# Performance work log

Measured on AMD Instinct MI355X. Metric: run time of the kernel, lower is better.

The kernel has to match this reference:

```python
import jax, jax.numpy as jnp
import numpy as np

N_NODES = 50000
N_EDGES = 800000
QRY = 128
KEY = 128
VAL = 128
HEADS = 8
HEAD_FEATS = VAL // HEADS
BN_EPS = 1e-5


def setup_inputs() -> dict:
    key = jax.random.key(0)
    ks = jax.random.split(key, 12)
    inp = {
        "ft_q": jax.random.normal(ks[0], (N_NODES, QRY), dtype=jnp.float32),
        "ft_k": jax.random.normal(ks[1], (N_NODES, KEY), dtype=jnp.float32),
        "src": jax.random.randint(ks[2], (N_EDGES,), 0, N_NODES, dtype=jnp.int32),
        "dst": jax.random.randint(ks[3], (N_EDGES,), 0, N_NODES, dtype=jnp.int32),
        # learned params
        "Wq": jax.random.normal(ks[4], (VAL, QRY), dtype=jnp.float32) / np.sqrt(QRY),
        "bq": jnp.zeros((VAL,), dtype=jnp.float32),
        "Wk": jax.random.normal(ks[5], (VAL, KEY), dtype=jnp.float32) / np.sqrt(KEY),
        "Wv": jax.random.normal(ks[6], (VAL, QRY), dtype=jnp.float32) / np.sqrt(QRY),
        "attn_e": jax.random.normal(ks[7], (VAL,), dtype=jnp.float32),
        "bn_q_g": jnp.ones((QRY,), dtype=jnp.float32),
        "bn_q_b": jnp.zeros((QRY,), dtype=jnp.float32),
        "bn_k_g": jnp.ones((KEY,), dtype=jnp.float32),
        "bn_k_b": jnp.zeros((KEY,), dtype=jnp.float32),
    }
    return inp


def _batch_norm(x, gamma, beta):
    # training-mode BatchNorm1d: normalize over batch dim
    mean = jnp.mean(x, axis=0, keepdims=True)
    var = jnp.var(x, axis=0, keepdims=True)
    return (x - mean) * jax.lax.rsqrt(var + BN_EPS) * gamma + beta


def reference(ft_q, ft_k, src, dst, Wq, bq, Wk, Wv, attn_e,
              bn_q_g, bn_q_b, bn_k_g, bn_k_b):
    ft_q = _batch_norm(ft_q, bn_q_g, bn_q_b)
    ft_k = _batch_norm(ft_k, bn_k_g, bn_k_b)

    q = ft_q @ Wq.T + bq                      # [N, VAL]
    k = ft_k @ Wk.T                           # [N, VAL]
    v = (ft_q @ Wv.T).reshape(-1, HEADS, HEAD_FEATS)  # [N, H, D]

    # u_add_v: per-edge e = q[src] + k[dst]
    e = q[src] + k[dst]                       # [E, VAL]
    e = (attn_e * jax.nn.sigmoid(e)).reshape(-1, HEADS, HEAD_FEATS).sum(-1)  # [E, H]

    # edge_softmax grouped by destination node
    m = jax.ops.segment_max(e, dst, num_segments=N_NODES)   # [N, H]
    ex = jnp.exp(e - m[dst])                                # [E, H]
    s = jax.ops.segment_sum(ex, dst, num_segments=N_NODES)  # [N, H]
    a = ex / s[dst]                                         # [E, H]

    # u_mul_e_sum: scatter-sum of v[src] * a over destination
    msg = v[src] * a[:, :, None]                            # [E, H, D]
    rst = jax.ops.segment_sum(msg, dst, num_segments=N_NODES)  # [N, H, D]
    return rst.reshape(-1, VAL)
```

## Files before the change

### kernel.cpp

```cpp
#include <hip/hip_runtime.h>

#define N_NODES 50000
#define N_EDGES 800000
#define FEATS 128
#define NCHUNK 196
#define CPAD 50176
#define GEMM_BX 196
#define GEMM_BLOCKS 392
#define SCAT_BLOCKS 3125
#define NTILE 782
#define NF_WAVES 8192
#define STAT_BLOCKS 512
#define HIST_BLOCKS 512
#define HSEG 128
#define ESEG 6250
#define HQ 12544
#define CPQ 49

typedef __attribute__((ext_vector_type(8))) short bf16x8;
typedef __attribute__((ext_vector_type(4))) float f32x4;
typedef union { uint4 u; bf16x8 v; } pack8;

__device__ __forceinline__ unsigned short f2bf(float f){
  unsigned u = __float_as_uint(f);
  u += 0x7FFF + ((u >> 16) & 1);
  return (unsigned short)(u >> 16);
}
__device__ __forceinline__ unsigned cvtpk(float lo, float hi){
  unsigned r;
  asm("v_cvt_pk_bf16_f32 %0, %1, %2" : "=v"(r) : "v"(lo), "v"(hi));
  return r;
}
__device__ __forceinline__ void unpack8(uint4 p, float* f){
  f[0]=__uint_as_float(p.x << 16); f[1]=__uint_as_float(p.x & 0xffff0000u);
  f[2]=__uint_as_float(p.y << 16); f[3]=__uint_as_float(p.y & 0xffff0000u);
  f[4]=__uint_as_float(p.z << 16); f[5]=__uint_as_float(p.z & 0xffff0000u);
  f[6]=__uint_as_float(p.w << 16); f[7]=__uint_as_float(p.w & 0xffff0000u);
}

__global__ __launch_bounds__(256) void stats_hist_kernel(
    const float* __restrict__ ftq, const float* __restrict__ ftk,
    float* __restrict__ sums, unsigned short* __restrict__ xqb,
    const int* __restrict__ dstE, unsigned short* __restrict__ rankE,
    unsigned short* __restrict__ hmat, unsigned short* __restrict__ ctot){
  __shared__ float red[4*FEATS];
  __shared__ unsigned lh[HQ/2];
  int tid = threadIdx.x, bid = blockIdx.x;
  if (bid < STAT_BLOCKS){
    for (int i = tid; i < 4*FEATS; i += 256) red[i] = 0.f;
    __syncthreads();
    int sub = tid >> 5, c4 = tid & 31;
    const float* Xs = (sub < 4) ? ftq : ftk;
    int so = (sub < 4) ? 0 : 2*FEATS;
    bool isq = (sub < 4);
    float a0=0,a1=0,a2=0,a3=0,b0=0,b1=0,b2=0,b3=0;
    #pragma unroll 4
    for (int r = bid*4 + (sub&3); r < N_NODES; r += STAT_BLOCKS*4){
      float4 x = *(const float4*)(Xs + (size_t)r*FEATS + c4*4);
      if (isq)
        *(uint2*)&xqb[(size_t)r*FEATS + c4*4] = make_uint2(cvtpk(x.x,x.y), cvtpk(x.z,x.w));
      a0+=x.x; b0+=x.x*x.x; a1+=x.y; b1+=x.y*x.y;
      a2+=x.z; b2+=x.z*x.z; a3+=x.w; b3+=x.w*x.w;
    }
    a0 += __shfl_xor(a0,32); a1 += __shfl_xor(a1,32);
    a2 += __shfl_xor(a2,32); a3 += __shfl_xor(a3,32);
    b0 += __shfl_xor(b0,32); b1 += __shfl_xor(b1,32);
    b2 += __shfl_xor(b2,32); b3 += __shfl_xor(b3,32);
    if ((tid & 63) < 32){
      int c0 = c4*4;
      atomicAdd(&red[so + c0+0], a0); atomicAdd(&red[so + c0+1], a1);
      atomicAdd(&red[so + c0+2], a2); atomicAdd(&red[so + c0+3], a3);
      atomicAdd(&red[so + FEATS + c0+0], b0); atomicAdd(&red[so + FEATS + c0+1], b1);
      atomicAdd(&red[so + FEATS + c0+2], b2); atomicAdd(&red[so + FEATS + c0+3], b3);
    }
    __syncthreads();
    for (int i = tid; i < 4*FEATS; i += 256) atomicAdd(&sums[i], red[i]);
  } else {
    int hb = bid - STAT_BLOCKS;
    int seg = hb >> 2, q = hb & 3;
    int dlo = q * HQ;
    for (int i = tid; i < HQ/2; i += 256) lh[i] = 0;
    __syncthreads();
    int e0 = seg * ESEG;
    for (int t = e0 + tid; t < e0 + ESEG; t += 256){
      int d = dstE[t] - dlo;
      if ((unsigned)d < (unsigned)HQ){
        unsigned sh = (d & 1) * 16;
        unsigned old = atomicAdd(&lh[d >> 1], 1u << sh);
        rankE[t] = (unsigned short)((old >> sh) & 0xffffu);
      }
    }
    __syncthreads();
    unsigned* row = (unsigned*)(hmat + (size_t)hb * HQ);
    for (int i = tid; i < HQ/2; i += 256) row[i] = lh[i];
    int wv = tid >> 6, ln = tid & 63;
    for (int c = wv; c < CPQ; c += 4){
      unsigned w0 = lh[c*128 + ln];
      unsigned w1 = lh[c*128 + 64 + ln];
      unsigned t = (w0 & 0xffffu) + (w0 >> 16) + (w1 & 0xffffu) + (w1 >> 16);
      #pragma unroll
      for (int o = 1; o < 64; o <<= 1) t += __shfl_xor((int)t, o);
      if (ln == 0) ctot[hb*CPQ + c] = (unsigned short)t;
    }
  }
}

__global__ __launch_bounds__(256) void colscan_fold_kernel(
    const unsigned short* __restrict__ hmat, unsigned short* __restrict__ hbase,
    int* __restrict__ loc, const unsigned short* __restrict__ ctot, int* __restrict__ bscan,
    const float* __restrict__ Wq, const float* __restrict__ bq,
    const float* __restrict__ Wk, const float* __restrict__ Wv,
    const float* __restrict__ gq, const float* __restrict__ bqn,
    const float* __restrict__ gk, const float* __restrict__ bkn,
    const float* __restrict__ sums,
    unsigned short* __restrict__ Wb, float* __restrict__ bias){
  __shared__ int s[256];
  int tid = threadIdx.x, bid = blockIdx.x;
  if (bid < NCHUNK){
    int q = bid / CPQ;
    int d = bid*256 + tid;
    int col = d - q*HQ;
    const unsigned short* hp = hmat + (size_t)q*HQ + col;
    unsigned short* bp = hbase + (size_t)q*HQ + col;
    int run = 0;
    #pragma unroll 8
    for (int sg = 0; sg < HSEG; sg++){
      int v = hp[(size_t)sg*4*HQ];
      bp[(size_t)sg*4*HQ] = (unsigned short)run;
      run += v;
    }
    s[tid] = run; __syncthreads();
    for (int dd = 1; dd < 256; dd <<= 1){
      int tv = (tid >= dd) ? s[tid-dd] : 0; __syncthreads();
      s[tid] += tv; __syncthreads();
    }
    loc[d] = s[tid] - run;
  } else if (bid == NCHUNK + 96){
    int v = 0;
    if (tid < NCHUNK){
      int q = tid / CPQ, cc = tid - q*CPQ;
      const unsigned short* cp = ctot + q*CPQ + cc;
      #pragma unroll 8
      for (int sg = 0; sg < HSEG; sg++) v += cp[(size_t)sg*4*CPQ];
    }
    s[tid] = v; __syncthreads();
    for (int dd = 1; dd < 256; dd <<= 1){
      int tv = (tid >= dd) ? s[tid-dd] : 0; __syncthreads();
      s[tid] += tv; __syncthreads();
    }
    if (tid < NCHUNK) bscan[tid] = s[tid] - v;
  } else {
    int wv = (bid - NCHUNK)*4 + (tid >> 6);
    int lane = tid & 63;
    int m = wv >> 7;
    int o = wv & 127;
    const float* Wsrc = (m==0) ? Wq : (m==1) ? Wv : Wk;
    const float* g   = (m==2) ? gk : gq;
    const float* bb  = (m==2) ? bkn : bqn;
    const float* s0  = (m==2) ? (sums + 2*FEATS) : sums;
    const float invN = 1.0f / (float)N_NODES;
    float acc = 0.f;
    unsigned short w2[2];
    int i0 = lane*2;
    #pragma unroll
    for (int t = 0; t < 2; t++){
      int i = i0 + t;
      float mean = s0[i]*invN;
      float var  = s0[FEATS+i]*invN - mean*mean;
      float rstd = rsqrtf(var + 1e-5f);
      float scale = g[i]*rstd;
      float shift = bb[i] - mean*scale;
      float w = Wsrc[o*FEATS + i];
      w2[t] = f2bf(w*scale);
      acc += shift*w;
    }
    ((unsigned*)Wb)[(m*FEATS*FEATS + o*FEATS + i0) >> 1] =
        (unsigned)w2[0] | ((unsigned)w2[1] << 16);
    #pragma unroll
    for (int off = 1; off < 64; off <<= 1) acc += __shfl_xor(acc, off);
    if (lane == 0) bias[m*FEATS + o] = acc + ((m==0) ? bq[o] : 0.f);
  }
}

__global__ __launch_bounds__(256) void scatter_kernel(
    const int* __restrict__ dstE, const int* __restrict__ srcE,
    const int* __restrict__ loc, const int* __restrict__ bscan,
    const unsigned short* __restrict__ rankE, const unsigned short* __restrict__ hbase,
    int* __restrict__ src_csr){
  int t = blockIdx.x*256 + threadIdx.x;
  int d = dstE[t];
  int seg = t / ESEG;
  int q = d / HQ;
  int base = (int)hbase[(size_t)(seg*4 + q)*HQ + (d - q*HQ)];
  src_csr[loc[d] + bscan[d >> 8] + base + (int)rankE[t]] = srcE[t];
}

__global__ __launch_bounds__(256) void gemm_kernel(
    const unsigned short* __restrict__ xqb, const float* __restrict__ ftk,
    const unsigned short* __restrict__ Wball, const float* __restrict__ biasall,
    unsigned short* __restrict__ qv, unsigned short* __restrict__ kb){
  __shared__ unsigned short Bs[2][FEATS][FEATS];
  int tid = threadIdx.x, bid = blockIdx.x;
  int isk = (bid >= GEMM_BX);
  int bx = isk ? bid - GEMM_BX : bid;
  int nplanes = isk ? 1 : 2;
  {
    for (int p = 0; p < nplanes; p++){
      int m = isk ? 2 : p;
      const uint4* srcp = (const uint4*)(Wball + m*FEATS*FEATS);
      for (int idx = tid; idx < FEATS*FEATS/8; idx += 256){
        int n = idx >> 4, ck = idx & 15;
        *(uint4*)&Bs[p][n][(ck ^ (n & 15))*8] = srcp[idx];
      }
    }
  }
  __syncthreads();
  int wave = tid >> 6, lane = tid & 63;
  int mrow = lane & 15, quad = lane >> 4;
  float bv[2][8];
  #pragma unroll
  for (int p = 0; p < 2; p++)
    #pragma unroll
    for (int ct = 0; ct < 8; ct++)
      bv[p][ct] = biasall[(isk ? 2 : p)*FEATS + ct*16 + mrow];
  uint4 cur[4], nxt[4];
  auto loadA = [&](uint4* buf, int t){
    int arow = t*64 + wave*16 + mrow;
    if (!isk){
      const unsigned short* xp = xqb + (size_t)arow*FEATS + quad*8;
      buf[0] = *(const uint4*)xp;
      buf[1] = *(const uint4*)(xp + 32);
      buf[2] = *(const uint4*)(xp + 64);
      buf[3] = *(const uint4*)(xp + 96);
    } else {
      bool rok = arow < N_NODES;
      const float* xp = ftk + (size_t)(rok ? arow : 0)*FEATS + quad*8;
      #pragma unroll
      for (int kt = 0; kt < 4; kt++){
        float4 x0 = *(const float4*)(xp + kt*32);
        float4 x1 = *(const float4*)(xp + kt*32 + 4);
        if (!rok){ x0 = make_float4(0.f,0.f,0.f,0.f); x1 = x0; }
        buf[kt].x = cvtpk(x0.x, x0.y); buf[kt].y = cvtpk(x0.z, x0.w);
        buf[kt].z = cvtpk(x1.x, x1.y); buf[kt].w = cvtpk(x1.z, x1.w);
      }
    }
  };
  loadA(cur, bx);
  for (int t = bx; t < NTILE; t += GEMM_BX){
    int tn = t + GEMM_BX;
    if (tn < NTILE) loadA(nxt, tn);
    f32x4 acc[2][8];
    #pragma unroll
    for (int p = 0; p < 2; p++)
      #pragma unroll
      for (int i = 0; i < 8; i++) acc[p][i] = (f32x4){0.f,0.f,0.f,0.f};
    #pragma unroll
    for (int kt = 0; kt < 4; kt++){
      pack8 a; a.u = cur[kt];
      #pragma unroll
      for (int ct = 0; ct < 8; ct++){
        bf16x8 b0 = *(bf16x8*)&Bs[0][ct*16 + mrow][((kt*4 + quad) ^ mrow)*8];
        acc[0][ct] = __builtin_amdgcn_mfma_f32_16x16x32_bf16(a.v, b0, acc[0][ct], 0, 0, 0);
      }
      if (!isk){
        #pragma unroll
        for (int ct = 0; ct < 8; ct++){
          bf16x8 b1 = *(bf16x8*)&Bs[1][ct*16 + mrow][((kt*4 + quad) ^ mrow)*8];
          acc[1][ct] = __builtin_amdgcn_mfma_f32_16x16x32_bf16(a.v, b1, acc[1][ct], 0, 0, 0);
        }
      }
    }
    int row0 = t*64;
    #pragma unroll
    for (int p = 0; p < 2; p++){
      if (isk && p) break;
      unsigned short* Out = isk ? kb : (qv + p*128);
      const int ostride = isk ? FEATS : 256;
      #pragma unroll
      for (int ct = 0; ct < 8; ct++){
        int col = ct*16 + mrow;
        #pragma unroll
        for (int v = 0; v < 4; v++){
          int orow = row0 + wave*16 + quad*4 + v;
          float sv = acc[p][ct][v] + bv[p][ct];
          float pf = __shfl_xor(sv, 1);
          if (!(mrow & 1) && orow < N_NODES)
            *(unsigned*)&Out[(size_t)orow*ostride + col] = cvtpk(sv, pf);
        }
      }
    }
    #pragma unroll
    for (int i = 0; i < 4; i++) cur[i] = nxt[i];
  }
}

__global__ __launch_bounds__(256) void node_fused_kernel(
    const unsigned short* __restrict__ qv, const unsigned short* __restrict__ kb,
    const float* __restrict__ attn, const int* __restrict__ src_csr,
    const int* __restrict__ loc, const int* __restrict__ bscan,
    float* __restrict__ out){
  int tid = threadIdx.x;
  int lane = tid & 63;
  int h = lane & 7, g = lane >> 3;
  int w = blockIdx.x*4 + (tid >> 6);
  const float L2E = 1.44269504f;
  float ar[16];
  {
    const uint4* ap = (const uint4*)(attn + h*16);
    uint4 a0 = ap[0], a1 = ap[1], a2 = ap[2], a3 = ap[3];
    ar[0]=__uint_as_float(a0.x); ar[1]=__uint_as_float(a0.y); ar[2]=__uint_as_float(a0.z); ar[3]=__uint_as_float(a0.w);
    ar[4]=__uint_as_float(a1.x); ar[5]=__uint_as_float(a1.y); ar[6]=__uint_as_float(a1.z); ar[7]=__uint_as_float(a1.w);
    ar[8]=__uint_as_float(a2.x); ar[9]=__uint_as_float(a2.y); ar[10]=__uint_as_float(a2.z); ar[11]=__uint_as_float(a2.w);
    ar[12]=__uint_as_float(a3.x); ar[13]=__uint_as_float(a3.y); ar[14]=__uint_as_float(a3.z); ar[15]=__uint_as_float(a3.w);
  }
  for (int n = w; n < N_NODES; n += NF_WAVES){
    int off0 = loc[n]   + bscan[n>>8];
    int off1 = loc[n+1] + bscan[(n+1)>>8];
    int deg = off1 - off0;
    if (deg == 0){
      ((float2*)(out + (size_t)n*FEATS))[lane] = make_float2(0.f, 0.f);
      continue;
    }
    float kf2[16];
    {
      const unsigned short* kr = kb + (size_t)n*FEATS + h*16;
      uint4 k0 = *(const uint4*)kr;
      uint4 k1 = *(const uint4*)(kr + 8);
      float kf[16]; unpack8(k0, kf); unpack8(k1, kf+8);
      #pragma unroll
      for (int i = 0; i < 16; i++) kf2[i] = -L2E * kf[i];
    }
    float ssum = 0.f;
    float acc[16];
    #pragma unroll
    for (int i = 0; i < 16; i++) acc[i] = 0.f;
    if (g < deg){
      int sA = src_csr[off0 + g];
      int jB = g + 8;
      int sB = (jB < deg) ? src_csr[off0 + jB] : sA;
      const unsigned short* pA = qv + (size_t)sA*256 + h*16;
      uint4 qa0 = *(const uint4*)pA;
      uint4 qa1 = *(const uint4*)(pA + 8);
      while (true){
        uint4 va0 = *(const uint4*)(pA + 128);
        uint4 va1 = *(const uint4*)(pA + 136);
        const unsigned short* pB = qv + (size_t)sB*256 + h*16;
        uint4 qb0 = *(const uint4*)pB;
        uint4 qb1 = *(const uint4*)(pB + 8);
        int jC = jB + 8;
        int sC = (jC < deg) ? src_csr[off0 + jC] : sB;
        float qf[16]; unpack8(qa0, qf); unpack8(qa1, qf+8);
        float ta = 0.f, tb = 0.f, tc = 0.f, td = 0.f;
        #pragma unroll
        for (int i = 0; i < 16; i += 4){
          float x0 = fmaf(qf[i+0], -L2E, kf2[i+0]);
          float x1 = fmaf(qf[i+1], -L2E, kf2[i+1]);
          float x2 = fmaf(qf[i+2], -L2E, kf2[i+2]);
          float x3 = fmaf(qf[i+3], -L2E, kf2[i+3]);
          ta = fmaf(ar[i+0], __builtin_amdgcn_rcpf(1.f + __builtin_amdgcn_exp2f(x0)), ta);
          tb = fmaf(ar[i+1], __builtin_amdgcn_rcpf(1.f + __builtin_amdgcn_exp2f(x1)), tb);
          tc = fmaf(ar[i+2], __builtin_amdgcn_rcpf(1.f + __builtin_amdgcn_exp2f(x2)), tc);
          td = fmaf(ar[i+3], __builtin_amdgcn_rcpf(1.f + __builtin_amdgcn_exp2f(x3)), td);
        }
        float t = (ta + tb) + (tc + td);
        float ex = __builtin_amdgcn_exp2f(t * L2E);
        ssum += ex;
        float vf[16]; unpack8(va0, vf); unpack8(va1, vf+8);
        #pragma unroll
        for (int i = 0; i < 16; i++) acc[i] = fmaf(ex, vf[i], acc[i]);
        if (jB >= deg) break;
        qa0 = qb0; qa1 = qb1; pA = pB;
        jB = jC; sB = sC;
      }
    }
    ssum += __shfl_xor(ssum, 8); ssum += __shfl_xor(ssum, 16); ssum += __shfl_xor(ssum, 32);
    #pragma unroll
    for (int i = 0; i < 16; i++){
      acc[i] += __shfl_xor(acc[i], 8);
      acc[i] += __shfl_xor(acc[i], 16);
      acc[i] += __shfl_xor(acc[i], 32);
    }
    if (g == 0){
      float inv_s = 1.f / ssum;
      float4* op = (float4*)(out + (size_t)n*FEATS + h*16);
      op[0] = make_float4(acc[0]*inv_s, acc[1]*inv_s, acc[2]*inv_s, acc[3]*inv_s);
      op[1] = make_float4(acc[4]*inv_s, acc[5]*inv_s, acc[6]*inv_s, acc[7]*inv_s);
      op[2] = make_float4(acc[8]*inv_s, acc[9]*inv_s, acc[10]*inv_s, acc[11]*inv_s);
      op[3] = make_float4(acc[12]*inv_s, acc[13]*inv_s, acc[14]*inv_s, acc[15]*inv_s);
    }
  }
}

extern "C" void kernel_launch(void* const* d_in, const int* in_sizes, int n_in,
                              void* d_out, int out_size, void* d_ws, size_t ws_size,
                              hipStream_t stream){
  (void)in_sizes; (void)n_in; (void)out_size; (void)ws_size;
  const float* ftq  = (const float*)d_in[0];
  const float* ftk  = (const float*)d_in[1];
  const int*   srcE = (const int*)d_in[2];
  const int*   dstE = (const int*)d_in[3];
  const float* Wq   = (const float*)d_in[4];
  const float* bq   = (const float*)d_in[5];
  const float* Wk   = (const float*)d_in[6];
  const float* Wv   = (const float*)d_in[7];
  const float* attn = (const float*)d_in[8];
  const float* gq   = (const float*)d_in[9];
  const float* bqn  = (const float*)d_in[10];
  const float* gk   = (const float*)d_in[11];
  const float* bkn  = (const float*)d_in[12];

  char* ws = (char*)d_ws;
  float* sums    = (float*)(ws + 0);
  int*   bscan   = (int*)(ws + 2048);
  int*   loc     = (int*)(ws + 4096);
  int*   src_csr = (int*)(ws + 204800);
  unsigned short* rankE = (unsigned short*)(ws + 3404800);
  unsigned short* hmat  = (unsigned short*)(ws + 5004800);
  unsigned short* hbase = (unsigned short*)(ws + 17849856);
  unsigned short* ctot  = (unsigned short*)(ws + 30694912);
  unsigned short* Wb    = (unsigned short*)(ws + 30745088);
  float* biasf   = (float*)(ws + 30843392);
  unsigned short* xqb = (unsigned short*)(ws + 30844928);
  unsigned short* qv  = (unsigned short*)(ws + 43689984);
  unsigned short* kb  = (unsigned short*)(ws + 69289984);
  float* out = (float*)d_out;

  hipMemsetAsync(ws, 0, 2048, stream);

  hipLaunchKernelGGL(stats_hist_kernel, dim3(STAT_BLOCKS + HIST_BLOCKS), dim3(256), 0, stream,
                     ftq, ftk, sums, xqb, dstE, rankE, hmat, ctot);
  hipLaunchKernelGGL(colscan_fold_kernel, dim3(NCHUNK + 97), dim3(256), 0, stream,
                     hmat, hbase, loc, ctot, bscan,
                     Wq, bq, Wk, Wv, gq, bqn, gk, bkn, sums, Wb, biasf);
  hipLaunchKernelGGL(scatter_kernel, dim3(SCAT_BLOCKS), dim3(256), 0, stream,
                     dstE, srcE, loc, bscan, rankE, hbase, src_csr);
  hipLaunchKernelGGL(gemm_kernel, dim3(GEMM_BLOCKS), dim3(256), 0, stream,
                     xqb, ftk, Wb, biasf, qv, kb);
  hipLaunchKernelGGL(node_fused_kernel, dim3(NF_WAVES/4), dim3(256), 0, stream,
                     qv, kb, attn, src_csr, loc, bscan, out);
}
```

Before: 259.5 us.

## Replace global stat atomics with per-block partials and use packed FP32 math

Statistics blocks now write per-block partial sums to a workspace buffer instead of doing global atomics. The fold kernel reduces the 256 partials itself, which removes the memset launch, and the stats block count is halved. Separately, the node-fused kernel's inner sigmoid-dot and value-accumulation loops now use v_pk_fma/v_pk_add/v_pk_mul on float pairs to cut VALU instruction count. The trade-off is a serial 256-step reduction loop per lane in the fold kernel, plus inline asm that may constrain the compiler's scheduling.

```diff
diff --git a/kernel.cpp b/kernel.cpp
--- a/kernel.cpp
+++ b/kernel.cpp
@@ -10,15 +10,17 @@
 #define SCAT_BLOCKS 3125
 #define NTILE 782
 #define NF_WAVES 8192
-#define STAT_BLOCKS 512
+#define STAT_BLOCKS 256
 #define HIST_BLOCKS 512
 #define HSEG 128
 #define ESEG 6250
 #define HQ 12544
 #define CPQ 49
+#define NPART 256
 
 typedef __attribute__((ext_vector_type(8))) short bf16x8;
 typedef __attribute__((ext_vector_type(4))) float f32x4;
+typedef __attribute__((ext_vector_type(2))) float f32x2;
 typedef union { uint4 u; bf16x8 v; } pack8;
 
 __device__ __forceinline__ unsigned short f2bf(float f){
@@ -31,16 +33,31 @@
   asm("v_cvt_pk_bf16_f32 %0, %1, %2" : "=v"(r) : "v"(lo), "v"(hi));
   return r;
 }
-__device__ __forceinline__ void unpack8(uint4 p, float* f){
-  f[0]=__uint_as_float(p.x << 16); f[1]=__uint_as_float(p.x & 0xffff0000u);
-  f[2]=__uint_as_float(p.y << 16); f[3]=__uint_as_float(p.y & 0xffff0000u);
-  f[4]=__uint_as_float(p.z << 16); f[5]=__uint_as_float(p.z & 0xffff0000u);
-  f[6]=__uint_as_float(p.w << 16); f[7]=__uint_as_float(p.w & 0xffff0000u);
+__device__ __forceinline__ f32x2 pk_fma(f32x2 a, f32x2 b, f32x2 c){
+  f32x2 d;
+  asm("v_pk_fma_f32 %0, %1, %2, %3" : "=v"(d) : "v"(a), "v"(b), "v"(c));
+  return d;
+}
+__device__ __forceinline__ f32x2 pk_add(f32x2 a, f32x2 b){
+  f32x2 d;
+  asm("v_pk_add_f32 %0, %1, %2" : "=v"(d) : "v"(a), "v"(b));
+  return d;
+}
+__device__ __forceinline__ f32x2 pk_mul(f32x2 a, f32x2 b){
+  f32x2 d;
+  asm("v_pk_mul_f32 %0, %1, %2" : "=v"(d) : "v"(a), "v"(b));
+  return d;
+}
+__device__ __forceinline__ void unpack8p(uint4 p, f32x2* f){
+  f[0].x=__uint_as_float(p.x << 16); f[0].y=__uint_as_float(p.x & 0xffff0000u);
+  f[1].x=__uint_as_float(p.y << 16); f[1].y=__uint_as_float(p.y & 0xffff0000u);
+  f[2].x=__uint_as_float(p.z << 16); f[2].y=__uint_as_float(p.z & 0xffff0000u);
+  f[3].x=__uint_as_float(p.w << 16); f[3].y=__uint_as_float(p.w & 0xffff0000u);
 }
 
 __global__ __launch_bounds__(256) void stats_hist_kernel(
     const float* __restrict__ ftq, const float* __restrict__ ftk,
-    float* __restrict__ sums, unsigned short* __restrict__ xqb,
+    float* __restrict__ psum, unsigned short* __restrict__ xqb,
     const int* __restrict__ dstE, unsigned short* __restrict__ rankE,
     unsigned short* __restrict__ hmat, unsigned short* __restrict__ ctot){
   __shared__ float red[4*FEATS];
@@ -74,7 +91,7 @@
       atomicAdd(&red[so + FEATS + c0+2], b2); atomicAdd(&red[so + FEATS + c0+3], b3);
     }
     __syncthreads();
-    for (int i = tid; i < 4*FEATS; i += 256) atomicAdd(&sums[i], red[i]);
+    for (int i = tid; i < 4*FEATS; i += 256) psum[(size_t)bid*512 + i] = red[i];
   } else {
     int hb = bid - STAT_BLOCKS;
     int seg = hb >> 2, q = hb & 3;
@@ -112,7 +129,7 @@
     const float* __restrict__ Wk, const float* __restrict__ Wv,
     const float* __restrict__ gq, const float* __restrict__ bqn,
     const float* __restrict__ gk, const float* __restrict__ bkn,
-    const float* __restrict__ sums,
+    const float* __restrict__ psum,
     unsigned short* __restrict__ Wb, float* __restrict__ bias){
   __shared__ int s[256];
   int tid = threadIdx.x, bid = blockIdx.x;
@@ -157,16 +174,25 @@
     const float* Wsrc = (m==0) ? Wq : (m==1) ? Wv : Wk;
     const float* g   = (m==2) ? gk : gq;
     const float* bb  = (m==2) ? bkn : bqn;
-    const float* s0  = (m==2) ? (sums + 2*FEATS) : sums;
+    int base = (m==2) ? 2*FEATS : 0;
     const float invN = 1.0f / (float)N_NODES;
+    int i0 = lane*2;
+    float2 sm = make_float2(0.f,0.f), sv = make_float2(0.f,0.f);
+    const float* pp = psum + base + i0;
+    for (int p = 0; p < NPART; p++){
+      float2 a = *(const float2*)(pp + (size_t)p*512);
+      float2 b = *(const float2*)(pp + (size_t)p*512 + FEATS);
+      sm.x += a.x; sm.y += a.y; sv.x += b.x; sv.y += b.y;
+    }
     float acc = 0.f;
     unsigned short w2[2];
-    int i0 = lane*2;
     #pragma unroll
     for (int t = 0; t < 2; t++){
+      float sms = t ? sm.y : sm.x;
+      float svs = t ? sv.y : sv.x;
       int i = i0 + t;
-      float mean = s0[i]*invN;
-      float var  = s0[FEATS+i]*invN - mean*mean;
+      float mean = sms*invN;
+      float var  = svs*invN - mean*mean;
       float rstd = rsqrtf(var + 1e-5f);
       float scale = g[i]*rstd;
       float shift = bb[i] - mean*scale;
@@ -304,14 +330,16 @@
   int h = lane & 7, g = lane >> 3;
   int w = blockIdx.x*4 + (tid >> 6);
   const float L2E = 1.44269504f;
-  float ar[16];
+  const f32x2 nL2 = {-L2E, -L2E};
+  const f32x2 one2 = {1.f, 1.f};
+  f32x2 arp[8];
   {
-    const uint4* ap = (const uint4*)(attn + h*16);
-    uint4 a0 = ap[0], a1 = ap[1], a2 = ap[2], a3 = ap[3];
-    ar[0]=__uint_as_float(a0.x); ar[1]=__uint_as_float(a0.y); ar[2]=__uint_as_float(a0.z); ar[3]=__uint_as_float(a0.w);
-    ar[4]=__uint_as_float(a1.x); ar[5]=__uint_as_float(a1.y); ar[6]=__uint_as_float(a1.z); ar[7]=__uint_as_float(a1.w);
-    ar[8]=__uint_as_float(a2.x); ar[9]=__uint_as_float(a2.y); ar[10]=__uint_as_float(a2.z); ar[11]=__uint_as_float(a2.w);
-    ar[12]=__uint_as_float(a3.x); ar[13]=__uint_as_float(a3.y); ar[14]=__uint_as_float(a3.z); ar[15]=__uint_as_float(a3.w);
+    const float4* ap = (const float4*)(attn + h*16);
+    float4 a0 = ap[0], a1 = ap[1], a2 = ap[2], a3 = ap[3];
+    arp[0].x=a0.x; arp[0].y=a0.y; arp[1].x=a0.z; arp[1].y=a0.w;
+    arp[2].x=a1.x; arp[2].y=a1.y; arp[3].x=a1.z; arp[3].y=a1.w;
+    arp[4].x=a2.x; arp[4].y=a2.y; arp[5].x=a2.z; arp[5].y=a2.w;
+    arp[6].x=a3.x; arp[6].y=a3.y; arp[7].x=a3.z; arp[7].y=a3.w;
   }
   for (int n = w; n < N_NODES; n += NF_WAVES){
     int off0 = loc[n]   + bscan[n>>8];
@@ -321,19 +349,19 @@
       ((float2*)(out + (size_t)n*FEATS))[lane] = make_float2(0.f, 0.f);
       continue;
     }
-    float kf2[16];
+    f32x2 kf2p[8];
     {
       const unsigned short* kr = kb + (size_t)n*FEATS + h*16;
       uint4 k0 = *(const uint4*)kr;
       uint4 k1 = *(const uint4*)(kr + 8);
-      float kf[16]; unpack8(k0, kf); unpack8(k1, kf+8);
-      #pragma unroll
-      for (int i = 0; i < 16; i++) kf2[i] = -L2E * kf[i];
+      f32x2 kp[8]; unpack8p(k0, kp); unpack8p(k1, kp+4);
+      #pragma unroll
+      for (int j = 0; j < 8; j++) kf2p[j] = pk_mul(kp[j], nL2);
     }
     float ssum = 0.f;
-    float acc[16];
-    #pragma unroll
-    for (int i = 0; i < 16; i++) acc[i] = 0.f;
+    f32x2 acc2[8];
+    #pragma unroll
+    for (int j = 0; j < 8; j++){ acc2[j].x = 0.f; acc2[j].y = 0.f; }
     if (g < deg){
       int sA = src_csr[off0 + g];
       int jB = g + 8;
@@ -349,25 +377,27 @@
         uint4 qb1 = *(const uint4*)(pB + 8);
         int jC = jB + 8;
         int sC = (jC < deg) ? src_csr[off0 + jC] : sB;
-        float qf[16]; unpack8(qa0, qf); unpack8(qa1, qf+8);
+        f32x2 qp[8]; unpack8p(qa0, qp); unpack8p(qa1, qp+4);
         float ta = 0.f, tb = 0.f, tc = 0.f, td = 0.f;
         #pragma unroll
-        for (int i = 0; i < 16; i += 4){
-          float x0 = fmaf(qf[i+0], -L2E, kf2[i+0]);
-          float x1 = fmaf(qf[i+1], -L2E, kf2[i+1]);
-          float x2 = fmaf(qf[i+2], -L2E, kf2[i+2]);
-          float x3 = fmaf(qf[i+3], -L2E, kf2[i+3]);
-          ta = fmaf(ar[i+0], __builtin_amdgcn_rcpf(1.f + __builtin_amdgcn_exp2f(x0)), ta);
-          tb = fmaf(ar[i+1], __builtin_amdgcn_rcpf(1.f + __builtin_amdgcn_exp2f(x1)), tb);
-          tc = fmaf(ar[i+2], __builtin_amdgcn_rcpf(1.f + __builtin_amdgcn_exp2f(x2)), tc);
-          td = fmaf(ar[i+3], __builtin_amdgcn_rcpf(1.f + __builtin_amdgcn_exp2f(x3)), td);
+        for (int j = 0; j < 8; j++){
+          f32x2 xs = pk_fma(qp[j], nL2, kf2p[j]);
+          f32x2 ep;
+          ep.x = __builtin_amdgcn_exp2f(xs.x);
+          ep.y = __builtin_amdgcn_exp2f(xs.y);
+          f32x2 dp = pk_add(ep, one2);
+          float sl = __builtin_amdgcn_rcpf(dp.x);
+          float sh = __builtin_amdgcn_rcpf(dp.y);
+          if (j & 1){ tc = fmaf(arp[j].x, sl, tc); td = fmaf(arp[j].y, sh, td); }
+          else      { ta = fmaf(arp[j].x, sl, ta); tb = fmaf(arp[j].y, sh, tb); }
         }
         float t = (ta + tb) + (tc + td);
         float ex = __builtin_amdgcn_exp2f(t * L2E);
         ssum += ex;
-        float vf[16]; unpack8(va0, vf); unpack8(va1, vf+8);
+        f32x2 exx; exx.x = ex; exx.y = ex;
+        f32x2 vp[8]; unpack8p(va0, vp); unpack8p(va1, vp+4);
         #pragma unroll
-        for (int i = 0; i < 16; i++) acc[i] = fmaf(ex, vf[i], acc[i]);
+        for (int j = 0; j < 8; j++) acc2[j] = pk_fma(exx, vp[j], acc2[j]);
         if (jB >= deg) break;
         qa0 = qb0; qa1 = qb1; pA = pB;
         jB = jC; sB = sC;
@@ -375,18 +405,21 @@
     }
     ssum += __shfl_xor(ssum, 8); ssum += __shfl_xor(ssum, 16); ssum += __shfl_xor(ssum, 32);
     #pragma unroll
-    for (int i = 0; i < 16; i++){
-      acc[i] += __shfl_xor(acc[i], 8);
-      acc[i] += __shfl_xor(acc[i], 16);
-      acc[i] += __shfl_xor(acc[i], 32);
+    for (int j = 0; j < 8; j++){
+      acc2[j].x += __shfl_xor(acc2[j].x, 8);
+      acc2[j].x += __shfl_xor(acc2[j].x, 16);
+      acc2[j].x += __shfl_xor(acc2[j].x, 32);
+      acc2[j].y += __shfl_xor(acc2[j].y, 8);
+      acc2[j].y += __shfl_xor(acc2[j].y, 16);
+      acc2[j].y += __shfl_xor(acc2[j].y, 32);
     }
     if (g == 0){
       float inv_s = 1.f / ssum;
       float4* op = (float4*)(out + (size_t)n*FEATS + h*16);
-      op[0] = make_float4(acc[0]*inv_s, acc[1]*inv_s, acc[2]*inv_s, acc[3]*inv_s);
-      op[1] = make_float4(acc[4]*inv_s, acc[5]*inv_s, acc[6]*inv_s, acc[7]*inv_s);
-      op[2] = make_float4(acc[8]*inv_s, acc[9]*inv_s, acc[10]*inv_s, acc[11]*inv_s);
-      op[3] = make_float4(acc[12]*inv_s, acc[13]*inv_s, acc[14]*inv_s, acc[15]*inv_s);
+      op[0] = make_float4(acc2[0].x*inv_s, acc2[0].y*inv_s, acc2[1].x*inv_s, acc2[1].y*inv_s);
+      op[1] = make_float4(acc2[2].x*inv_s, acc2[2].y*inv_s, acc2[3].x*inv_s, acc2[3].y*inv_s);
+      op[2] = make_float4(acc2[4].x*inv_s, acc2[4].y*inv_s, acc2[5].x*inv_s, acc2[5].y*inv_s);
+      op[3] = make_float4(acc2[6].x*inv_s, acc2[6].y*inv_s, acc2[7].x*inv_s, acc2[7].y*inv_s);
     }
   }
 }
@@ -410,28 +443,27 @@
   const float* bkn  = (const float*)d_in[12];
 
   char* ws = (char*)d_ws;
-  float* sums    = (float*)(ws + 0);
-  int*   bscan   = (int*)(ws + 2048);
-  int*   loc     = (int*)(ws + 4096);
-  int*   src_csr = (int*)(ws + 204800);
-  unsigned short* rankE = (unsigned short*)(ws + 3404800);
-  unsigned short* hmat  = (unsigned short*)(ws + 5004800);
-  unsigned short* hbase = (unsigned short*)(ws + 17849856);
-  unsigned short* ctot  = (unsigned short*)(ws + 30694912);
-  unsigned short* Wb    = (unsigned short*)(ws + 30745088);
-  float* biasf   = (float*)(ws + 30843392);
-  unsigned short* xqb = (unsigned short*)(ws + 30844928);
-  unsigned short* qv  = (unsigned short*)(ws + 43689984);
-  unsigned short* kb  = (unsigned short*)(ws + 69289984);
+  float* psum    = (float*)(ws + 0);
+  int*   bscan   = (int*)(ws + 524288);
+  int*   loc     = (int*)(ws + 525312);
+  int*   src_csr = (int*)(ws + 726016);
+  unsigned short* rankE = (unsigned short*)(ws + 3926016);
+  unsigned short* hmat  = (unsigned short*)(ws + 5526016);
+  unsigned short* hbase = (unsigned short*)(ws + 18371072);
+  unsigned short* ctot  = (unsigned short*)(ws + 31216128);
+  unsigned short* Wb    = (unsigned short*)(ws + 31266304);
+  float* biasf   = (float*)(ws + 31364608);
+  unsigned short* xqb = (unsigned short*)(ws + 31366144);
+  unsigned short* qv  = (unsigned short*)(ws + 44211200);
+  unsigned short* kb  = (unsigned short*)(ws + 69811200);
   float* out = (float*)d_out;
 
-  hipMemsetAsync(ws, 0, 2048, stream);
 
   hipLaunchKernelGGL(stats_hist_kernel, dim3(STAT_BLOCKS + HIST_BLOCKS), dim3(256), 0, stream,
-                     ftq, ftk, sums, xqb, dstE, rankE, hmat, ctot);
+                     ftq, ftk, psum, xqb, dstE, rankE, hmat, ctot);
   hipLaunchKernelGGL(colscan_fold_kernel, dim3(NCHUNK + 97), dim3(256), 0, stream,
                      hmat, hbase, loc, ctot, bscan,
-                     Wq, bq, Wk, Wv, gq, bqn, gk, bkn, sums, Wb, biasf);
+                     Wq, bq, Wk, Wv, gq, bqn, gk, bkn, psum, Wb, biasf);
   hipLaunchKernelGGL(scatter_kernel, dim3(SCAT_BLOCKS), dim3(256), 0, stream,
                      dstE, srcE, loc, bscan, rankE, hbase, src_csr);
   hipLaunchKernelGGL(gemm_kernel, dim3(GEMM_BLOCKS), dim3(256), 0, stream,
```

Result: slower. 271.0 us (+4.5%).
